# Kernel tuning notes

Measured on AMD Instinct MI355X. Metric: run time of the kernel, lower is better.

The kernel has to match this reference:

```python
import jax, jax.numpy as jnp
import numpy as np

N_NODES = 50000
N_EDGES = 400000
N_GRAPHS = 256
HID = 128
FEAT_IN, POS_IN, EDGE_IN = 64, 16, 16
N_LAYERS = 4


def _lin(x, w, b):
    return x @ w.T + b


def setup_inputs() -> dict:
    key = jax.random.key(0)
    ks = iter(jax.random.split(key, 64))
    s = 0.05

    def w(shape):
        return (jax.random.normal(next(ks), shape, dtype=jnp.float32) * s)

    inp = {
        "h": jax.random.normal(next(ks), (N_NODES, FEAT_IN), dtype=jnp.float32),
        "e": jax.random.normal(next(ks), (N_EDGES, EDGE_IN), dtype=jnp.float32),
        "p": jax.random.normal(next(ks), (N_NODES, POS_IN), dtype=jnp.float32),
        "edge_index": jax.random.randint(next(ks), (2, N_EDGES), 0, N_NODES),
        "batch": jnp.sort(jax.random.randint(next(ks), (N_NODES,), 0, N_GRAPHS)),
        # embeddings
        "h_embed_w": w((HID, FEAT_IN)), "h_embed_b": w((HID,)),
        "e_embed_w": w((HID, EDGE_IN)), "e_embed_b": w((HID,)),
        "p_embed_w": w((HID, POS_IN)), "p_embed_b": w((HID,)),
        # per-layer params, stacked over layers
        "hu_w": w((N_LAYERS, HID, 5 * HID)), "hu_b": w((N_LAYERS, HID)),
        "eu_w": w((N_LAYERS, HID, 3 * HID)), "eu_b": w((N_LAYERS, HID)),
        "pu_w": w((N_LAYERS, HID, 3 * HID)), "pu_b": w((N_LAYERS, HID)),
        "hagg_w": w((N_LAYERS, HID, 2 * HID)), "hagg_b": w((N_LAYERS, HID)),
        "pagg_w": w((N_LAYERS, HID, 2 * HID)), "pagg_b": w((N_LAYERS, HID)),
        # readout MLP
        "r1_w": w((HID, 2 * HID)), "r1_b": w((HID,)),
        "r2_w": w((HID // 2, HID)), "r2_b": w((HID // 2,)),
        "r3_w": w((1, HID // 2)), "r3_b": w((1,)),
    }
    return inp


def reference(h, e, p, edge_index, batch,
              h_embed_w, h_embed_b, e_embed_w, e_embed_b, p_embed_w, p_embed_b,
              hu_w, hu_b, eu_w, eu_b, pu_w, pu_b,
              hagg_w, hagg_b, pagg_w, pagg_b,
              r1_w, r1_b, r2_w, r2_b, r3_w, r3_b):
    send, rec = edge_index[0], edge_index[1]
    N = h.shape[0]

    h = _lin(h, h_embed_w, h_embed_b)
    e = _lin(e, e_embed_w, e_embed_b)
    p = _lin(p, p_embed_w, p_embed_b)

    for l in range(N_LAYERS):
        hp_send = jnp.concatenate((h[send], p[send]), axis=1)  # [E, 2H]
        hp_rec = jnp.concatenate((h[rec], p[rec]), axis=1)     # [E, 2H]
        h_msg = _lin(jnp.concatenate((hp_send, hp_rec, e), axis=1), hu_w[l], hu_b[l])
        h_msg_agg = jax.ops.segment_sum(h_msg, rec, num_segments=N)
        h = _lin(jnp.concatenate((h, h_msg_agg), axis=1), hagg_w[l], hagg_b[l])
        e = _lin(jnp.concatenate((h[send], h[rec], e), axis=1), eu_w[l], eu_b[l])
        p_msg = _lin(jnp.concatenate((p[send], p[rec], e), axis=1), pu_w[l], pu_b[l])
        p_msg_agg = jax.ops.segment_sum(p_msg, rec, num_segments=N)
        p = _lin(jnp.concatenate((p, p_msg_agg), axis=1), pagg_w[l], pagg_b[l])

    h_agg = jax.ops.segment_sum(h, batch, num_segments=N_GRAPHS)
    p_agg = jax.ops.segment_sum(p, batch, num_segments=N_GRAPHS)
    hep = jnp.concatenate((h_agg, p_agg), axis=1)
    x = jax.nn.relu(_lin(hep, r1_w, r1_b))
    x = jax.nn.relu(_lin(x, r2_w, r2_b))
    out = _lin(x, r3_w, r3_b).squeeze(-1)  # [N_GRAPHS]
    return (out, p)
```

## Files before the change

kernel.cpp:

```cpp
#include <hip/hip_runtime.h>

typedef __attribute__((ext_vector_type(8))) short bf16x8;
typedef __attribute__((ext_vector_type(4))) float f32x4;
typedef __attribute__((ext_vector_type(4))) unsigned short us4;

__device__ __forceinline__ float b2f(unsigned short h) {
  union { unsigned int u; float f; } v; v.u = ((unsigned int)h) << 16; return v.f;
}
__device__ __forceinline__ unsigned short f2b(float f) {
  union { float f; unsigned int u; } v; v.f = f;
  unsigned int r = v.u + 0x7fffu + ((v.u >> 16) & 1u);
  return (unsigned short)(r >> 16);
}

__global__ void f2b_kernel(const float* __restrict__ in, unsigned short* __restrict__ out, int n4) {
  int i = blockIdx.x * blockDim.x + threadIdx.x;
  int stride = gridDim.x * blockDim.x;
  for (; i < n4; i += stride) {
    float4 v = reinterpret_cast<const float4*>(in)[i];
    us4 o;
    o[0] = f2b(v.x); o[1] = f2b(v.y); o[2] = f2b(v.z); o[3] = f2b(v.w);
    reinterpret_cast<us4*>(out)[i] = o;
  }
}

__launch_bounds__(256)
__global__ void compose_w(const float* __restrict__ hg, const float* __restrict__ hu,
                          const float* __restrict__ pg, const float* __restrict__ pu,
                          const float* __restrict__ hub, const float* __restrict__ pub,
                          unsigned short* __restrict__ wh, unsigned short* __restrict__ wp,
                          float* __restrict__ bh, float* __restrict__ bp) {
  __shared__ float As[128][129];
  __shared__ float Bs[128][36];
  __shared__ float bvs[128];
  const int l = blockIdx.x >> 5, t = blockIdx.x & 31;
  const float* A; const float* B; const float* bv; unsigned short* W; float* bo;
  int lda, ldb, K2, ldw, cbase;
  if (t < 20) {
    A = hg + (size_t)l * 128 * 256; lda = 256;
    B = hu + (size_t)l * 128 * 640; ldb = 640; K2 = 640;
    W = wh + (size_t)l * 128 * 768; ldw = 768;
    bv = hub + l * 128; bo = bh + l * 128; cbase = t * 32;
  } else {
    A = pg + (size_t)l * 128 * 256; lda = 256;
    B = pu + (size_t)l * 128 * 384; ldb = 384; K2 = 384;
    W = wp + (size_t)l * 128 * 512; ldw = 512;
    bv = pub + l * 128; bo = bp + l * 128; cbase = (t - 20) * 32;
  }
  const int tid = threadIdx.x;
  for (int idx = tid; idx < 128 * 128; idx += 256) {
    int r = idx >> 7, c = idx & 127;
    As[r][c] = A[r * lda + 128 + c];
  }
  for (int idx = tid; idx < 128 * 32; idx += 256) {
    int m = idx >> 5, c = idx & 31;
    Bs[m][c] = B[m * ldb + cbase + c];
  }
  if (tid < 128) bvs[tid] = bv[tid];
  __syncthreads();
  const int o = tid & 127, g = tid >> 7;
  float acc[16];
#pragma unroll
  for (int j = 0; j < 16; ++j) acc[j] = 0.f;
  for (int m = 0; m < 128; ++m) {
    float a = As[o][m];
#pragma unroll
    for (int j4 = 0; j4 < 4; ++j4) {
      float4 b4 = *reinterpret_cast<const float4*>(&Bs[m][g * 16 + j4 * 4]);
      acc[j4 * 4 + 0] += a * b4.x; acc[j4 * 4 + 1] += a * b4.y;
      acc[j4 * 4 + 2] += a * b4.z; acc[j4 * 4 + 3] += a * b4.w;
    }
  }
#pragma unroll
  for (int j4 = 0; j4 < 4; ++j4) {
    us4 ov;
    ov[0] = f2b(acc[j4 * 4 + 0]); ov[1] = f2b(acc[j4 * 4 + 1]);
    ov[2] = f2b(acc[j4 * 4 + 2]); ov[3] = f2b(acc[j4 * 4 + 3]);
    *reinterpret_cast<us4*>(&W[(long)o * ldw + cbase + g * 16 + j4 * 4]) = ov;
  }
  if (cbase == 0) {
    for (int idx = tid; idx < 128 * 128; idx += 256) {
      int oo = idx >> 7, m = idx & 127;
      W[(long)oo * ldw + K2 + m] = f2b(A[oo * lda + m]);
    }
    if (tid < 128) {
      float s = 0.f;
      for (int m = 0; m < 128; ++m) s += As[tid][m] * bvs[m];
      bo[tid] = s;
    }
  }
}

template<int K>
__launch_bounds__(256)
__global__ void embed_fast(const float* __restrict__ in, const float* __restrict__ w,
                           const float* __restrict__ b, unsigned short* __restrict__ out,
                           long M, int ostride, int ocoloff, const float* __restrict__ degB,
                           unsigned short* __restrict__ out2, const float* __restrict__ scaleF) {
  __shared__ float wT[K][129];
  __shared__ float xt[16 * K];
  const int tid = threadIdx.x;
  const int col = tid & 127;
  const int half = tid >> 7;
  for (int idx = tid; idx < 128 * K; idx += 256) {
    int c = idx / K, k = idx % K;
    wT[k][c] = w[idx];
  }
  __syncthreads();
  float wreg[K];
#pragma unroll
  for (int k = 0; k < K; ++k) wreg[k] = wT[k][col];
  const float bcol = b[col];

  for (long r0 = (long)blockIdx.x * 16; r0 < M; r0 += (long)gridDim.x * 16) {
    __syncthreads();
    const float4* src4 = reinterpret_cast<const float4*>(in + r0 * K);
    const int n4 = 16 * K / 4;
    if (r0 + 16 <= M) {
      for (int i = tid; i < n4; i += 256)
        reinterpret_cast<float4*>(xt)[i] = src4[i];
    } else {
      int rem = (int)((M - r0) * K) / 4;
      for (int i = tid; i < n4; i += 256) {
        float4 z = {0.f, 0.f, 0.f, 0.f};
        reinterpret_cast<float4*>(xt)[i] = (i < rem) ? src4[i] : z;
      }
    }
    __syncthreads();
#pragma unroll
    for (int rr = 0; rr < 8; ++rr) {
      long row = r0 + half * 8 + rr;
      if (row >= M) break;
      const float* xr = &xt[(half * 8 + rr) * K];
      float acc = bcol * (degB ? degB[row] : 1.0f);
#pragma unroll
      for (int k4 = 0; k4 < K / 4; ++k4) {
        float4 xv = reinterpret_cast<const float4*>(xr)[k4];
        acc += xv.x * wreg[k4 * 4] + xv.y * wreg[k4 * 4 + 1] +
               xv.z * wreg[k4 * 4 + 2] + xv.w * wreg[k4 * 4 + 3];
      }
      long o = row * ostride + ocoloff + col;
      out[o] = f2b(acc);
      if (out2) out2[o] = f2b(acc * scaleF[row]);
    }
  }
}

__global__ void count_deg(const int* __restrict__ rec, int* __restrict__ deg, int E) {
  int i = blockIdx.x * blockDim.x + threadIdx.x;
  if (i < E) atomicAdd(&deg[rec[i]], 1);
}

__global__ void scan_blk(const int* __restrict__ deg, int* __restrict__ tmp,
                         int* __restrict__ blkSum, int N) {
  __shared__ int ts[256];
  const int b = blockIdx.x, t = threadIdx.x;
  const int base = b * 1024 + t * 4;
  int v0 = (base + 0 < N) ? deg[base + 0] : 0;
  int v1 = (base + 1 < N) ? deg[base + 1] : 0;
  int v2 = (base + 2 < N) ? deg[base + 2] : 0;
  int v3 = (base + 3 < N) ? deg[base + 3] : 0;
  int tsum = v0 + v1 + v2 + v3;
  ts[t] = tsum;
  __syncthreads();
  for (int off = 1; off < 256; off <<= 1) {
    int x = (t >= off) ? ts[t - off] : 0;
    __syncthreads();
    ts[t] += x;
    __syncthreads();
  }
  int texcl = ts[t] - tsum;
  if (base + 0 < N) tmp[base + 0] = texcl;
  if (base + 1 < N) tmp[base + 1] = texcl + v0;
  if (base + 2 < N) tmp[base + 2] = texcl + v0 + v1;
  if (base + 3 < N) tmp[base + 3] = texcl + v0 + v1 + v2;
  if (t == 255) blkSum[b] = ts[255];
}

__global__ void scan_top(int* __restrict__ blkSum, int nb) {
  __shared__ int s[64];
  int t = threadIdx.x;
  if (t < nb) s[t] = blkSum[t];
  __syncthreads();
  if (t == 0) {
    int run = 0;
    for (int i = 0; i < nb; ++i) { int x = s[i]; s[i] = run; run += x; }
  }
  __syncthreads();
  if (t < nb) blkSum[t] = s[t];
}

__global__ void scan_fix(const int* __restrict__ deg, int* __restrict__ row_ptr,
                         const int* __restrict__ blkOff, int* __restrict__ cursor,
                         float* __restrict__ degF, int N, int E) {
  const int b = blockIdx.x, t = threadIdx.x;
  const int base = b * 1024 + t * 4;
  const int off = blkOff[b];
#pragma unroll
  for (int k = 0; k < 4; ++k) {
    int i = base + k;
    if (i < N) {
      int v = row_ptr[i] + off;
      row_ptr[i] = v;
      cursor[i] = v;
      degF[i] = (float)deg[i];
    }
  }
  if (b == 0 && t == 0) row_ptr[N] = E;
}

__global__ void scatter_perm(const int* __restrict__ rec, const int* __restrict__ send,
                             int* __restrict__ cursor, int* __restrict__ perm,
                             int* __restrict__ sendP, int E) {
  int i = blockIdx.x * blockDim.x + threadIdx.x;
  if (i < E) {
    int pos = atomicAdd(&cursor[rec[i]], 1);
    perm[pos] = i;
    sendP[pos] = send[i];
  }
}

__global__ void segsum_raw(const float* __restrict__ eraw, const int* __restrict__ row_ptr,
                           const int* __restrict__ perm, float* __restrict__ out16, int N) {
  int sub = threadIdx.x >> 4;
  int f = threadIdx.x & 15;
  int r = blockIdx.x * 16 + sub;
  if (r >= N) return;
  int j0 = row_ptr[r], j1 = row_ptr[r + 1];
  float s0 = 0.f, s1 = 0.f;
  int j = j0;
  for (; j + 2 <= j1; j += 2) {
    int e0 = perm[j], e1 = perm[j + 1];
    s0 += eraw[(long)e0 * 16 + f];
    s1 += eraw[(long)e1 * 16 + f];
  }
  if (j < j1) s0 += eraw[(long)perm[j] * 16 + f];
  out16[(long)r * 16 + f] = s0 + s1;
}

__launch_bounds__(256)
__global__ void gather_sum256(const unsigned short* __restrict__ src,
                              const int* __restrict__ row_ptr, const int* __restrict__ sendP,
                              unsigned short* __restrict__ dst, int N) {
  const int wid = threadIdx.x >> 6, lane = threadIdx.x & 63;
  const int r = blockIdx.x * 4 + wid;
  if (r >= N) return;
  const int j0 = row_ptr[r], j1 = row_ptr[r + 1];
  const int off = lane * 4;
  float a0 = 0.f, a1 = 0.f, a2 = 0.f, a3 = 0.f;
  int j = j0;
  for (; j + 2 <= j1; j += 2) {
    int i0 = sendP[j], i1 = sendP[j + 1];
    us4 x = *reinterpret_cast<const us4*>(&src[(long)i0 * 256 + off]);
    us4 y = *reinterpret_cast<const us4*>(&src[(long)i1 * 256 + off]);
    a0 += b2f(x[0]) + b2f(y[0]); a1 += b2f(x[1]) + b2f(y[1]);
    a2 += b2f(x[2]) + b2f(y[2]); a3 += b2f(x[3]) + b2f(y[3]);
  }
  if (j < j1) {
    us4 x = *reinterpret_cast<const us4*>(&src[(long)sendP[j] * 256 + off]);
    a0 += b2f(x[0]); a1 += b2f(x[1]); a2 += b2f(x[2]); a3 += b2f(x[3]);
  }
  us4 o;
  o[0] = f2b(a0); o[1] = f2b(a1); o[2] = f2b(a2); o[3] = f2b(a3);
  *reinterpret_cast<us4*>(&dst[(long)r * 256 + off]) = o;
}

__launch_bounds__(256)
__global__ void gather_sum128(const unsigned short* __restrict__ src, int col,
                              const int* __restrict__ row_ptr, const int* __restrict__ sendP,
                              unsigned short* __restrict__ dst, int N) {
  const int wid = threadIdx.x >> 6, lane = threadIdx.x & 63;
  const int r = blockIdx.x * 4 + wid;
  if (r >= N) return;
  const int j0 = row_ptr[r], j1 = row_ptr[r + 1];
  const int half = lane >> 5;
  const int c = lane & 31;
  const int off = col + c * 4;
  float a0 = 0.f, a1 = 0.f, a2 = 0.f, a3 = 0.f;
  float b0 = 0.f, b1 = 0.f, b2 = 0.f, b3 = 0.f;
  int j = j0 + half;
  for (; j + 2 < j1; j += 4) {
    int i0 = sendP[j], i1 = sendP[j + 2];
    us4 x = *reinterpret_cast<const us4*>(&src[(long)i0 * 256 + off]);
    us4 y = *reinterpret_cast<const us4*>(&src[(long)i1 * 256 + off]);
    a0 += b2f(x[0]); a1 += b2f(x[1]); a2 += b2f(x[2]); a3 += b2f(x[3]);
    b0 += b2f(y[0]); b1 += b2f(y[1]); b2 += b2f(y[2]); b3 += b2f(y[3]);
  }
  if (j < j1) {
    us4 x = *reinterpret_cast<const us4*>(&src[(long)sendP[j] * 256 + off]);
    a0 += b2f(x[0]); a1 += b2f(x[1]); a2 += b2f(x[2]); a3 += b2f(x[3]);
  }
  a0 += b0; a1 += b1; a2 += b2; a3 += b3;
  a0 += __shfl_xor(a0, 32); a1 += __shfl_xor(a1, 32);
  a2 += __shfl_xor(a2, 32); a3 += __shfl_xor(a3, 32);
  if (half == 0) {
    us4 o;
    o[0] = f2b(a0); o[1] = f2b(a1); o[2] = f2b(a2); o[3] = f2b(a3);
    *reinterpret_cast<us4*>(&dst[(long)r * 256 + off]) = o;
  }
}

__launch_bounds__(256, 3)
__global__ void gemm_mp(int M, int nsrc, int strides, int coloffs,
                        const unsigned short* __restrict__ sp0, const unsigned short* __restrict__ sp1,
                        const unsigned short* __restrict__ sp2, const unsigned short* __restrict__ sp3,
                        const unsigned short* __restrict__ sp4, const unsigned short* __restrict__ sp5,
                        const unsigned short* __restrict__ Wb,
                        const float* __restrict__ bdeg, const float* __restrict__ bone,
                        const float* __restrict__ degF,
                        unsigned short* __restrict__ outB, int ostride, int ocoloff,
                        unsigned short* __restrict__ outB2, float* __restrict__ outF) {
  __shared__ __align__(16) unsigned short ldsW[8 * 64 * 8];
  const int tid = threadIdx.x;
  const int wid = tid >> 6, lane = tid & 63;
  const int K = nsrc * 128;
  const long rowBase = (long)blockIdx.x * 128 + wid * 32;
  const int lq = lane >> 4;
  const int lr = lane & 15;

  int rowD[2];
#pragma unroll
  for (int am = 0; am < 2; ++am) {
    long e = rowBase + am * 16 + lr;
    if (e >= M) e = M - 1;
    rowD[am] = (int)e;
  }

  f32x4 acc[2][8];
#pragma unroll
  for (int i = 0; i < 2; ++i)
#pragma unroll
    for (int j = 0; j < 8; ++j) acc[i][j] = 0.f;

  for (int si = 0; si < nsrc; ++si) {
    const unsigned short* sp = (si == 0) ? sp0 : (si == 1) ? sp1 : (si == 2) ? sp2
                              : (si == 3) ? sp3 : (si == 4) ? sp4 : sp5;
    const long astride = (long)(((strides >> (si * 4)) & 15) * 128);
    const int acoloff = ((coloffs >> (si * 4)) & 15) * 128;
#pragma unroll
    for (int sub = 0; sub < 4; ++sub) {
      const int koff = acoloff + sub * 32 + lq * 8;
      bf16x8 a[2];
#pragma unroll
      for (int am = 0; am < 2; ++am)
        a[am] = *reinterpret_cast<const bf16x8*>(&sp[(long)rowD[am] * astride + koff]);
      __syncthreads();
#pragma unroll
      for (int it = 0; it < 2; ++it) {
        int idx = tid + it * 256;
        int t = idx >> 6, l = idx & 63;
        int n = t * 16 + (l & 15);
        int kk = si * 128 + sub * 32 + ((l >> 4) * 8);
        *reinterpret_cast<bf16x8*>(&ldsW[idx * 8]) =
            *reinterpret_cast<const bf16x8*>(&Wb[(long)n * K + kk]);
      }
      __syncthreads();
#pragma unroll
      for (int n = 0; n < 8; ++n) {
        bf16x8 b = *reinterpret_cast<const bf16x8*>(&ldsW[(n * 64 + lane) * 8]);
#pragma unroll
        for (int am = 0; am < 2; ++am)
          acc[am][n] = __builtin_amdgcn_mfma_f32_16x16x32_bf16(a[am], b, acc[am][n], 0, 0, 0);
      }
    }
  }

  float bd[8], bo[8];
#pragma unroll
  for (int n = 0; n < 8; ++n) {
    bd[n] = bdeg ? bdeg[n * 16 + lr] : 0.f;
    bo[n] = bone ? bone[n * 16 + lr] : 0.f;
  }

#pragma unroll
  for (int am = 0; am < 2; ++am) {
#pragma unroll
    for (int r = 0; r < 4; ++r) {
      long row = rowBase + am * 16 + lq * 4 + r;
      if (row < M) {
        float d = degF[row];
        long ob = row * ostride + ocoloff;
#pragma unroll
        for (int n = 0; n < 8; ++n) {
          float v = acc[am][n][r] + bd[n] * d + bo[n];
          outB[ob + n * 16 + lr] = f2b(v);
          if (outB2) outB2[ob + n * 16 + lr] = f2b(v * d);
          if (outF) outF[row * 128 + n * 16 + lr] = v;
        }
      }
    }
  }
}

__global__ void readout_agg(const unsigned short* __restrict__ hp,
                            const int* __restrict__ batch, float* __restrict__ hep, int N) {
  int col = threadIdx.x;
  int n0 = blockIdx.x * 128;
  int n1 = n0 + 128; if (n1 > N) n1 = N;
  float sum = 0.f; int curg = -1;
  for (int n = n0; n < n1; ++n) {
    int g = batch[n];
    if (g != curg) {
      if (curg >= 0) unsafeAtomicAdd(&hep[(long)curg * 256 + col], sum);
      curg = g; sum = 0.f;
    }
    sum += b2f(hp[(long)n * 256 + col]);
  }
  if (curg >= 0) unsafeAtomicAdd(&hep[(long)curg * 256 + col], sum);
}

__global__ void mlp_kernel(const float* __restrict__ hep,
                           const float* __restrict__ r1w, const float* __restrict__ r1b,
                           const float* __restrict__ r2w, const float* __restrict__ r2b,
                           const float* __restrict__ r3w, const float* __restrict__ r3b,
                           float* __restrict__ out) {
  int g = blockIdx.x, t = threadIdx.x;
  __shared__ float x[256];
  __shared__ float y[128];
  __shared__ float z[64];
  x[t] = hep[(long)g * 256 + t];
  x[t + 128] = hep[(long)g * 256 + 128 + t];
  __syncthreads();
  float s = r1b[t];
  for (int k = 0; k < 256; ++k) s += r1w[t * 256 + k] * x[k];
  y[t] = fmaxf(s, 0.f);
  __syncthreads();
  if (t < 64) {
    float s2 = r2b[t];
    for (int k = 0; k < 128; ++k) s2 += r2w[t * 128 + k] * y[k];
    z[t] = fmaxf(s2, 0.f);
  }
  __syncthreads();
  if (t == 0) {
    float s3 = r3b[0];
    for (int k = 0; k < 64; ++k) s3 += r3w[k] * z[k];
    out[g] = s3;
  }
}

extern "C" void kernel_launch(void* const* d_in, const int* in_sizes, int n_in,
                              void* d_out, int out_size, void* d_ws, size_t ws_size,
                              hipStream_t stream) {
  const float* h_in = (const float*)d_in[0];
  const float* e_in = (const float*)d_in[1];
  const float* p_in = (const float*)d_in[2];
  const int* ei = (const int*)d_in[3];
  const int* batch = (const int*)d_in[4];
  const float* he_w = (const float*)d_in[5];  const float* he_b = (const float*)d_in[6];
  const float* ee_w = (const float*)d_in[7];  const float* ee_b = (const float*)d_in[8];
  const float* pe_w = (const float*)d_in[9];  const float* pe_b = (const float*)d_in[10];
  const float* hu_w = (const float*)d_in[11]; const float* hu_b = (const float*)d_in[12];
  const float* eu_w = (const float*)d_in[13]; const float* eu_b = (const float*)d_in[14];
  const float* pu_w = (const float*)d_in[15]; const float* pu_b = (const float*)d_in[16];
  const float* hg_w = (const float*)d_in[17]; const float* hg_b = (const float*)d_in[18];
  const float* pg_w = (const float*)d_in[19]; const float* pg_b = (const float*)d_in[20];
  const float* r1w = (const float*)d_in[21];  const float* r1b = (const float*)d_in[22];
  const float* r2w = (const float*)d_in[23];  const float* r2b = (const float*)d_in[24];
  const float* r3w = (const float*)d_in[25];  const float* r3b = (const float*)d_in[26];

  const int N = 50000, E = 400000, G = 256;
  const int* send = ei;
  const int* rec = ei + E;

  char* ws = (char*)d_ws;
  size_t off = 0;
  auto alloc = [&](size_t bytes) {
    void* pp = ws + off;
    off += (bytes + 255) & ~(size_t)255;
    return pp;
  };
  unsigned short* hp  = (unsigned short*)alloc((size_t)N * 256 * 2);
  unsigned short* dhp = (unsigned short*)alloc((size_t)N * 256 * 2);
  unsigned short* gHP = (unsigned short*)alloc((size_t)N * 256 * 2);
  unsigned short* sT  = (unsigned short*)alloc((size_t)N * 128 * 2);
  float* segsumF = (float*)alloc((size_t)N * 16 * 4);
  int* deg = (int*)alloc((size_t)N * 4);
  int* row_ptr = (int*)alloc((size_t)(N + 1) * 4);
  int* cursor = (int*)alloc((size_t)N * 4);
  int* blkSum = (int*)alloc((size_t)64 * 4);
  int* perm = (int*)alloc((size_t)E * 4);
  int* sendP = (int*)alloc((size_t)E * 4);
  float* degF = (float*)alloc((size_t)N * 4);
  float* hep = (float*)alloc((size_t)G * 256 * 4);
  unsigned short* w_h2 = (unsigned short*)alloc((size_t)4 * 128 * 768 * 2);
  unsigned short* w_p2 = (unsigned short*)alloc((size_t)4 * 128 * 512 * 2);
  unsigned short* w_eu = (unsigned short*)alloc((size_t)4 * 128 * 384 * 2);
  float* bh1 = (float*)alloc((size_t)4 * 128 * 4);
  float* bp1 = (float*)alloc((size_t)4 * 128 * 4);
  (void)ws_size; (void)n_in; (void)in_sizes; (void)out_size;

  f2b_kernel<<<192, 256, 0, stream>>>(eu_w, w_eu, 4 * 128 * 384 / 4);
  compose_w<<<128, 256, 0, stream>>>(hg_w, hu_w, pg_w, pu_w, hu_b, pu_b, w_h2, w_p2, bh1, bp1);

  const int nb = (N + 1023) / 1024;
  hipMemsetAsync(deg, 0, (size_t)N * 4, stream);
  count_deg<<<(E + 255) / 256, 256, 0, stream>>>(rec, deg, E);
  scan_blk<<<nb, 256, 0, stream>>>(deg, row_ptr, blkSum, N);
  scan_top<<<1, 64, 0, stream>>>(blkSum, nb);
  scan_fix<<<nb, 256, 0, stream>>>(deg, row_ptr, blkSum, cursor, degF, N, E);
  scatter_perm<<<(E + 255) / 256, 256, 0, stream>>>(rec, send, cursor, perm, sendP, E);

  embed_fast<64><<<3125, 256, 0, stream>>>(h_in, he_w, he_b, hp, N, 256, 0, nullptr, dhp, degF);
  embed_fast<16><<<3125, 256, 0, stream>>>(p_in, pe_w, pe_b, hp, N, 256, 128, nullptr, dhp, degF);
  segsum_raw<<<(N + 15) / 16, 256, 0, stream>>>(e_in, row_ptr, perm, segsumF, N);
  embed_fast<16><<<3125, 256, 0, stream>>>(segsumF, ee_w, ee_b, sT, N, 128, 0, degF, nullptr, nullptr);

  gather_sum256<<<(N + 3) / 4, 256, 0, stream>>>(hp, row_ptr, sendP, gHP, N);

  float* pOut = (float*)d_out + 256;
  const int gridN = (N + 127) / 128;
  const int gridG = (N + 3) / 4;

  for (int l = 0; l < 4; ++l) {
    gemm_mp<<<gridN, 256, 0, stream>>>(N, 6, 0x212222, 0x001010,
        gHP, gHP, dhp, dhp, sT, hp,
        w_h2 + (size_t)l * 128 * 768, bh1 + l * 128, hg_b + l * 128, degF,
        hp, 256, 0, dhp, nullptr);
    gather_sum128<<<gridG, 256, 0, stream>>>(hp, 0, row_ptr, sendP, gHP, N);
    gemm_mp<<<gridN, 256, 0, stream>>>(N, 3, 0x122, 0x000,
        gHP, dhp, sT, nullptr, nullptr, nullptr,
        w_eu + (size_t)l * 128 * 384, eu_b + l * 128, nullptr, degF,
        sT, 128, 0, nullptr, nullptr);
    gemm_mp<<<gridN, 256, 0, stream>>>(N, 4, 0x2122, 0x1011,
        gHP, dhp, sT, hp, nullptr, nullptr,
        w_p2 + (size_t)l * 128 * 512, bp1 + l * 128, pg_b + l * 128, degF,
        hp, 256, 128, (l < 3) ? dhp : nullptr, (l == 3) ? pOut : nullptr);
    if (l < 3)
      gather_sum128<<<gridG, 256, 0, stream>>>(hp, 128, row_ptr, sendP, gHP, N);
  }

  hipMemsetAsync(hep, 0, (size_t)G * 256 * 4, stream);
  readout_agg<<<(N + 127) / 128, 256, 0, stream>>>(hp, batch, hep, N);
  mlp_kernel<<<G, 128, 0, stream>>>(hep, r1w, r1b, r2w, r2b, r3w, r3b, (float*)d_out);
}
```

Measured before the change: 713.8 us.

## Load GEMM weight fragments directly from global memory and unroll gather loops deeper

The message-passing GEMM no longer stages weight tiles through shared memory with two barriers per K-step. Each lane now loads its B fragments straight from global memory, relying on L1/L2 hits because every wave reads the same small weight matrix. The launch-bounds occupancy hint goes from 3 to 4 blocks. Both gather-sum kernels unroll their neighbor loops to four rows per iteration so more loads are in flight. The cost is redundant global and L1 weight traffic across waves and possible register pressure at the higher occupancy target.

Result: slower. 955.3 us (+33.8%).

```diff
diff --git a/kernel.cpp b/kernel.cpp
--- a/kernel.cpp
+++ b/kernel.cpp
@@ -249,14 +249,18 @@
   const int off = lane * 4;
   float a0 = 0.f, a1 = 0.f, a2 = 0.f, a3 = 0.f;
   int j = j0;
-  for (; j + 2 <= j1; j += 2) {
-    int i0 = sendP[j], i1 = sendP[j + 1];
+  for (; j + 4 <= j1; j += 4) {
+    int i0 = sendP[j], i1 = sendP[j + 1], i2 = sendP[j + 2], i3 = sendP[j + 3];
     us4 x = *reinterpret_cast<const us4*>(&src[(long)i0 * 256 + off]);
     us4 y = *reinterpret_cast<const us4*>(&src[(long)i1 * 256 + off]);
-    a0 += b2f(x[0]) + b2f(y[0]); a1 += b2f(x[1]) + b2f(y[1]);
-    a2 += b2f(x[2]) + b2f(y[2]); a3 += b2f(x[3]) + b2f(y[3]);
-  }
-  if (j < j1) {
+    us4 z = *reinterpret_cast<const us4*>(&src[(long)i2 * 256 + off]);
+    us4 w = *reinterpret_cast<const us4*>(&src[(long)i3 * 256 + off]);
+    a0 += b2f(x[0]) + b2f(y[0]) + b2f(z[0]) + b2f(w[0]);
+    a1 += b2f(x[1]) + b2f(y[1]) + b2f(z[1]) + b2f(w[1]);
+    a2 += b2f(x[2]) + b2f(y[2]) + b2f(z[2]) + b2f(w[2]);
+    a3 += b2f(x[3]) + b2f(y[3]) + b2f(z[3]) + b2f(w[3]);
+  }
+  for (; j < j1; ++j) {
     us4 x = *reinterpret_cast<const us4*>(&src[(long)sendP[j] * 256 + off]);
     a0 += b2f(x[0]); a1 += b2f(x[1]); a2 += b2f(x[2]); a3 += b2f(x[3]);
   }
@@ -279,6 +283,17 @@
   float a0 = 0.f, a1 = 0.f, a2 = 0.f, a3 = 0.f;
   float b0 = 0.f, b1 = 0.f, b2 = 0.f, b3 = 0.f;
   int j = j0 + half;
+  for (; j + 6 < j1; j += 8) {
+    int i0 = sendP[j], i1 = sendP[j + 2], i2 = sendP[j + 4], i3 = sendP[j + 6];
+    us4 x = *reinterpret_cast<const us4*>(&src[(long)i0 * 256 + off]);
+    us4 y = *reinterpret_cast<const us4*>(&src[(long)i1 * 256 + off]);
+    us4 z = *reinterpret_cast<const us4*>(&src[(long)i2 * 256 + off]);
+    us4 w = *reinterpret_cast<const us4*>(&src[(long)i3 * 256 + off]);
+    a0 += b2f(x[0]) + b2f(z[0]); a1 += b2f(x[1]) + b2f(z[1]);
+    a2 += b2f(x[2]) + b2f(z[2]); a3 += b2f(x[3]) + b2f(z[3]);
+    b0 += b2f(y[0]) + b2f(w[0]); b1 += b2f(y[1]) + b2f(w[1]);
+    b2 += b2f(y[2]) + b2f(w[2]); b3 += b2f(y[3]) + b2f(w[3]);
+  }
   for (; j + 2 < j1; j += 4) {
     int i0 = sendP[j], i1 = sendP[j + 2];
     us4 x = *reinterpret_cast<const us4*>(&src[(long)i0 * 256 + off]);
@@ -300,7 +315,7 @@
   }
 }
 
-__launch_bounds__(256, 3)
+__launch_bounds__(256, 4)
 __global__ void gemm_mp(int M, int nsrc, int strides, int coloffs,
                         const unsigned short* __restrict__ sp0, const unsigned short* __restrict__ sp1,
                         const unsigned short* __restrict__ sp2, const unsigned short* __restrict__ sp3,
@@ -310,7 +325,6 @@
                         const float* __restrict__ degF,
                         unsigned short* __restrict__ outB, int ostride, int ocoloff,
                         unsigned short* __restrict__ outB2, float* __restrict__ outF) {
-  __shared__ __align__(16) unsigned short ldsW[8 * 64 * 8];
   const int tid = threadIdx.x;
   const int wid = tid >> 6, lane = tid & 63;
   const int K = nsrc * 128;
@@ -332,6 +346,8 @@
 #pragma unroll
     for (int j = 0; j < 8; ++j) acc[i][j] = 0.f;
 
+  const unsigned short* wlane = Wb + (long)lr * K + lq * 8;
+
   for (int si = 0; si < nsrc; ++si) {
     const unsigned short* sp = (si == 0) ? sp0 : (si == 1) ? sp1 : (si == 2) ? sp2
                               : (si == 3) ? sp3 : (si == 4) ? sp4 : sp5;
@@ -344,23 +360,18 @@
 #pragma unroll
       for (int am = 0; am < 2; ++am)
         a[am] = *reinterpret_cast<const bf16x8*>(&sp[(long)rowD[am] * astride + koff]);
-      __syncthreads();
-#pragma unroll
-      for (int it = 0; it < 2; ++it) {
-        int idx = tid + it * 256;
-        int t = idx >> 6, l = idx & 63;
-        int n = t * 16 + (l & 15);
-        int kk = si * 128 + sub * 32 + ((l >> 4) * 8);
-        *reinterpret_cast<bf16x8*>(&ldsW[idx * 8]) =
-            *reinterpret_cast<const bf16x8*>(&Wb[(long)n * K + kk]);
-      }
-      __syncthreads();
-#pragma unroll
-      for (int n = 0; n < 8; ++n) {
-        bf16x8 b = *reinterpret_cast<const bf16x8*>(&ldsW[(n * 64 + lane) * 8]);
-#pragma unroll
-        for (int am = 0; am < 2; ++am)
-          acc[am][n] = __builtin_amdgcn_mfma_f32_16x16x32_bf16(a[am], b, acc[am][n], 0, 0, 0);
+      const unsigned short* wk = wlane + si * 128 + sub * 32;
+#pragma unroll
+      for (int g = 0; g < 2; ++g) {
+        bf16x8 bfr[4];
+#pragma unroll
+        for (int n = 0; n < 4; ++n)
+          bfr[n] = *reinterpret_cast<const bf16x8*>(wk + (long)(g * 4 + n) * 16 * K);
+#pragma unroll
+        for (int n = 0; n < 4; ++n) {
+          acc[0][g * 4 + n] = __builtin_amdgcn_mfma_f32_16x16x32_bf16(a[0], bfr[n], acc[0][g * 4 + n], 0, 0, 0);
+          acc[1][g * 4 + n] = __builtin_amdgcn_mfma_f32_16x16x32_bf16(a[1], bfr[n], acc[1][g * 4 + n], 0, 0, 0);
+        }
       }
     }
   }
```
